# Kernel tuning notes

Hardware: AMD Instinct MI355X
Metric: run time of the kernel (lower is better)

## Reference

```python
import jax, jax.numpy as jnp
import numpy as np

K = 8          # circulant block size
H = 16         # heads


def circ_linear(x, w, b):
    """Block-circulant linear. x: [..., in], w: [p, q, K] (first column of each
    KxK circulant block), b: [p*K]. y[p] = sum_q circ(w[p,q]) @ x_block[q],
    computed as circular convolution via rFFT."""
    q = w.shape[1]
    xb = x.reshape(x.shape[:-1] + (q, K))            # [..., q, K]
    Fx = jnp.fft.rfft(xb, axis=-1)                    # [..., q, K//2+1]
    Fw = jnp.fft.rfft(w, axis=-1)                     # [p, q, K//2+1]
    Fy = jnp.einsum('pqf,...qf->...pf', Fw, Fx)
    y = jnp.fft.irfft(Fy, n=K, axis=-1)               # [..., p, K]
    return y.reshape(x.shape[:-1] + (-1,)) + b


def setup_inputs() -> dict:
    key = jax.random.key(0)
    ks = jax.random.split(key, 9)
    B, N, D = 2, 1024, 1024
    p = q = D // K
    std = 1.0 / np.sqrt(D)
    mk = lambda k: jax.random.normal(k, (p, q, K), dtype=jnp.float32) * std
    mb = lambda k: jax.random.normal(k, (D,), dtype=jnp.float32) * 0.01
    x = jax.random.normal(ks[0], (B, N, D), dtype=jnp.float32)
    # causal mask: True = masked out
    mask = (~jnp.tril(jnp.ones((N, N), dtype=bool)))[None, None]  # [1,1,N,N]
    return {
        'x': x, 'mask': mask,
        'wq': mk(ks[1]), 'bq': mb(ks[2]),
        'wk': mk(ks[3]), 'bk': mb(ks[4]),
        'wv': mk(ks[5]), 'bv': mb(ks[6]),
        'wo': mk(ks[7]), 'bo': mb(ks[8]),
    }


def reference(x, mask, wq, bq, wk, bk, wv, bv, wo, bo):
    B, N, D = x.shape
    dh = D // H
    heads = lambda a: a.reshape(B, N, H, dh).transpose(0, 2, 1, 3)  # [B,H,N,dh]
    qh = heads(circ_linear(x, wq, bq))
    kh = heads(circ_linear(x, wk, bk))
    vh = heads(circ_linear(x, wv, bv))
    attn = jnp.einsum('bhnd,bhmd->bhnm', qh, kh)
    attn = jnp.where(mask, -jnp.inf, attn)
    probs = jax.nn.softmax(attn / jnp.sqrt(jnp.float32(dh)), axis=-1)
    out = jnp.einsum('bhnm,bhmd->bhnd', probs, vh)
    out = out.transpose(0, 2, 1, 3).reshape(B, N, D)
    return circ_linear(out, wo, bo)
```

## Files before the change

kernel.cpp:

```cpp
#include <hip/hip_runtime.h>
#include <hip/hip_bf16.h>

#define DIM   1024
#define NSEQ  1024
#define BATCH 2
#define NHEAD 16
#define DH    64

typedef unsigned short u16;
typedef __attribute__((ext_vector_type(8))) short  short8;
typedef __attribute__((ext_vector_type(4))) float  f32x4;
typedef __attribute__((ext_vector_type(8))) unsigned short u16x8;
typedef __attribute__((ext_vector_type(4))) unsigned short u16x4;

#define EXP_SCALE 0.18033688011112042f
#define SLOT 4352

__device__ __forceinline__ u16 f2bf(float f) {
  union { float f; unsigned u; } v; v.f = f;
  unsigned r = v.u + 0x7FFFu + ((v.u >> 16) & 1u);
  return (u16)(r >> 16);
}

#define GLD(src, dst)                                                          \
  __builtin_amdgcn_global_load_lds(                                           \
      (const __attribute__((address_space(1))) void*)(src),                   \
      (__attribute__((address_space(3))) void*)(dst), 16, 0, 0)

__global__ __launch_bounds__(256) void prep_bf16(
    const float* __restrict__ wq, const float* __restrict__ wk,
    const float* __restrict__ wv, const float* __restrict__ wo,
    const float* __restrict__ x,
    u16* __restrict__ Wd, u16* __restrict__ Xb) {
  const int bid = blockIdx.x;
  if (bid < 2048) {
    const int z = bid >> 9;
    const float* w = (z == 0) ? wq : (z == 1) ? wk : (z == 2) ? wv : wo;
    u16* out = Wd + (size_t)z * DIM * DIM;
    const int idx8 = (bid & 511) * 256 + threadIdx.x;
    const int r = idx8 >> 7;
    const int q = idx8 & 127;
    const int p = r >> 3, a = r & 7;
    const float* wrow = w + (size_t)(p * 128 + q) * 8;
    const float4 w0 = *(const float4*)(wrow);
    const float4 w1 = *(const float4*)(wrow + 4);
    const float wv8[8] = {w0.x, w0.y, w0.z, w0.w, w1.x, w1.y, w1.z, w1.w};
    u16x8 o;
#pragma unroll
    for (int j = 0; j < 8; ++j) o[j] = f2bf(wv8[(a - j) & 7]);
    ((u16x8*)out)[idx8] = o;
  } else {
    const int i = (bid - 2048) * 256 + threadIdx.x;
    const float4 a = ((const float4*)x)[2 * i];
    const float4 b = ((const float4*)x)[2 * i + 1];
    u16x8 o;
    o[0] = f2bf(a.x); o[1] = f2bf(a.y); o[2] = f2bf(a.z); o[3] = f2bf(a.w);
    o[4] = f2bf(b.x); o[5] = f2bf(b.y); o[6] = f2bf(b.z); o[7] = f2bf(b.w);
    ((u16x8*)Xb)[i] = o;
  }
}

__global__ __launch_bounds__(256, 2) void gemm_qkv(
    const u16* __restrict__ A, const u16* __restrict__ Wd,
    const float* __restrict__ bq, const float* __restrict__ bk,
    const float* __restrict__ bv,
    u16* __restrict__ Qb, u16* __restrict__ Kb, u16* __restrict__ Vt) {
  __shared__ u16 As[2][64 * 64];
  __shared__ u16 Bs[2][3 * 64 * 64];

  const int tid  = threadIdx.x;
  const int w    = tid >> 6, lane = tid & 63;
  const int nb   = blockIdx.x * 64;
  const int mb   = blockIdx.y * 64;

  f32x4 acc[3][2][2] = {};

  const int m0 = (w >> 1) * 32, n0 = (w & 1) * 32;
  const int lr = lane & 15, lg = lane >> 4;
  const int lsw = lr & 7;

#define STAGE(buf, k0)                                                         \
  do {                                                                         \
    _Pragma("unroll")                                                          \
    for (int i = 0; i < 2; ++i) {                                              \
      const int bc = i * 256 + w * 64;                                         \
      const int c  = bc + lane;                                                \
      const int row = c >> 3, js = (c & 7) ^ (row & 7);                        \
      GLD(A + (size_t)(mb + row) * DIM + (k0) + js * 8, As[buf] + bc * 8);     \
    }                                                                          \
    _Pragma("unroll")                                                          \
    for (int i = 0; i < 6; ++i) {                                              \
      const int bc = i * 256 + w * 64;                                         \
      const int c  = bc + lane;                                                \
      const int z  = c >> 9, ci = c & 511;                                     \
      const int row = ci >> 3, js = (ci & 7) ^ (row & 7);                      \
      GLD(Wd + (size_t)z * DIM * DIM + (size_t)(nb + row) * DIM + (k0) + js * 8,\
          Bs[buf] + bc * 8);                                                   \
    }                                                                          \
  } while (0)

  STAGE(0, 0);
  __syncthreads();
  int cur = 0;
  for (int k0 = 0; k0 < DIM; k0 += 64) {
    if (k0 + 64 < DIM) STAGE(cur ^ 1, k0 + 64);

#pragma unroll
    for (int kk = 0; kk < 2; ++kk) {
      const int sw = ((kk * 4 + lg) ^ lsw) * 8;
      short8 a[2], b[3][2];
#pragma unroll
      for (int mi = 0; mi < 2; ++mi)
        a[mi] = *(const short8*)&As[cur][(m0 + mi * 16 + lr) * 64 + sw];
#pragma unroll
      for (int z = 0; z < 3; ++z)
#pragma unroll
        for (int ni = 0; ni < 2; ++ni)
          b[z][ni] = *(const short8*)
              &Bs[cur][z * 4096 + (n0 + ni * 16 + lr) * 64 + sw];
#pragma unroll
      for (int z = 0; z < 3; ++z)
#pragma unroll
        for (int mi = 0; mi < 2; ++mi)
#pragma unroll
          for (int ni = 0; ni < 2; ++ni)
            acc[z][mi][ni] = __builtin_amdgcn_mfma_f32_16x16x32_bf16(
                a[mi], b[z][ni], acc[z][mi][ni], 0, 0, 0);
    }

    __syncthreads();
    cur ^= 1;
  }
#undef STAGE

  const int col = lane & 15, rq4 = (lane >> 4) * 4;

#pragma unroll
  for (int z = 0; z < 2; ++z) {
    u16* C = z ? Kb : Qb;
    const float* bias = z ? bk : bq;
#pragma unroll
    for (int ni = 0; ni < 2; ++ni) {
      const int gc = nb + n0 + ni * 16 + col;
      const float bb = bias[gc];
#pragma unroll
      for (int mi = 0; mi < 2; ++mi) {
        const size_t rbase = (size_t)(mb + m0 + mi * 16 + rq4) * DIM + gc;
#pragma unroll
        for (int j = 0; j < 4; ++j)
          C[rbase + (size_t)j * DIM] = f2bf(acc[z][mi][ni][j] + bb);
      }
    }
  }
  {
    const int b = mb >> 10;
    const int h = blockIdx.x;
    const int nbase = (mb & (NSEQ - 1)) + m0;
#pragma unroll
    for (int ni = 0; ni < 2; ++ni) {
      const int dh = n0 + ni * 16 + col;
      const float bb = bv[nb + dh];
      u16* vrow = Vt + ((size_t)(b * NHEAD + h) * DH + dh) * NSEQ;
#pragma unroll
      for (int mi = 0; mi < 2; ++mi) {
        const int nn = nbase + mi * 16 + rq4;
        u16x4 o;
#pragma unroll
        for (int j = 0; j < 4; ++j) o[j] = f2bf(acc[2][mi][ni][j] + bb);
        *(u16x4*)(vrow + nn) = o;
      }
    }
  }
}

__global__ __launch_bounds__(256, 2) void gemm_o(
    const u16* __restrict__ A, const u16* __restrict__ W,
    const float* __restrict__ bias, float* __restrict__ C) {
  __shared__ u16 As[2][64 * 64];
  __shared__ u16 Bs[2][64 * 64];

  const int tid  = threadIdx.x;
  const int w    = tid >> 6, lane = tid & 63;
  const int mb   = blockIdx.y * 64, nb = blockIdx.x * 64;

  f32x4 acc[2][2] = {};

  const int m0 = (w >> 1) * 32, n0 = (w & 1) * 32;
  const int lr = lane & 15, lg = lane >> 4;
  const int lsw = lr & 7;

#define STAGE(buf, k0)                                                         \
  do {                                                                         \
    _Pragma("unroll")                                                          \
    for (int i = 0; i < 2; ++i) {                                              \
      const int bc = i * 256 + w * 64;                                         \
      const int c  = bc + lane;                                                \
      const int row = c >> 3, js = (c & 7) ^ (row & 7);                        \
      GLD(A + (size_t)(mb + row) * DIM + (k0) + js * 8, As[buf] + bc * 8);     \
      GLD(W + (size_t)(nb + row) * DIM + (k0) + js * 8, Bs[buf] + bc * 8);     \
    }                                                                          \
  } while (0)

  STAGE(0, 0);
  __syncthreads();
  int cur = 0;
  for (int k0 = 0; k0 < DIM; k0 += 64) {
    if (k0 + 64 < DIM) STAGE(cur ^ 1, k0 + 64);

#pragma unroll
    for (int kk = 0; kk < 2; ++kk) {
      const int sw = ((kk * 4 + lg) ^ lsw) * 8;
      short8 a[2], b[2];
#pragma unroll
      for (int mi = 0; mi < 2; ++mi)
        a[mi] = *(const short8*)&As[cur][(m0 + mi * 16 + lr) * 64 + sw];
#pragma unroll
      for (int ni = 0; ni < 2; ++ni)
        b[ni] = *(const short8*)&Bs[cur][(n0 + ni * 16 + lr) * 64 + sw];
#pragma unroll
      for (int mi = 0; mi < 2; ++mi)
#pragma unroll
        for (int ni = 0; ni < 2; ++ni)
          acc[mi][ni] = __builtin_amdgcn_mfma_f32_16x16x32_bf16(
              a[mi], b[ni], acc[mi][ni], 0, 0, 0);
    }

    __syncthreads();
    cur ^= 1;
  }
#undef STAGE

  const int col = lane & 15, rq = (lane >> 4) * 4;
#pragma unroll
  for (int ni = 0; ni < 2; ++ni) {
    const int gc = nb + n0 + ni * 16 + col;
    const float bv = bias[gc];
#pragma unroll
    for (int mi = 0; mi < 2; ++mi) {
      const size_t rbase = (size_t)(mb + m0 + mi * 16 + rq) * DIM + gc;
#pragma unroll
      for (int j = 0; j < 4; ++j)
        C[rbase + (size_t)j * DIM] = acc[mi][ni][j] + bv;
    }
  }
}

__global__ __launch_bounds__(256, 4) void attn_split(
    const u16* __restrict__ Qg, const u16* __restrict__ Kg,
    const u16* __restrict__ Vt, float* __restrict__ Part,
    u16* __restrict__ AOb) {
  const int bid = blockIdx.x;
  const int s   = bid >> 3;
  const int g   = (bid & 7) * 4 + s / 40;
  const int b   = g >> 4, h = g & 15;
  int idx = s % 40, qt = 0, cc = 0;
  for (int t = 15; t >= 0; --t) {
    const int nc = (t >> 2) + 1;
    if (idx < nc) { qt = t; cc = idx; break; }
    idx -= nc;
  }
  const int tid = threadIdx.x;
  const int w  = tid >> 6, l = tid & 63;
  const int lr = l & 15, lg = l >> 4;

  __shared__ u16 Klds[4][64 * 64];
  __shared__ u16 Vlds[4][64 * 64];
  __shared__ u16 Plds[4][16 * 64];

  const int qg = qt * 64 + w * 16 + lr;
  const size_t base_bh = (size_t)b * NSEQ * DIM + (size_t)h * DH;
  const size_t vt_bh   = (size_t)(b * NHEAD + h) * DH * NSEQ;

  short8 qf[2];
#pragma unroll
  for (int c = 0; c < 2; ++c)
    qf[c] = *(const short8*)(Qg + base_bh + (size_t)qg * DIM + c * 32 + lg * 8);

  f32x4 acc_o[4] = {};
  float m_run = -1e30f, l_run = 0.f;
  char* pbase = (char*)Plds[w];
  const int psw = (lr & 7) << 4;

  const int srow8 = l >> 3;
  const int sj    = l & 7;

  const int kt0 = cc * 4;
  const int nt  = min(kt0 + 4, qt + 1) - kt0;

#pragma unroll
  for (int t = 0; t < 4; ++t) {
    if (t < nt) {
      const int kt = kt0 + t;
#pragma unroll
      for (int i = 0; i < 2; ++i) {
        const int cb  = w * 2 + i;
        const int row = cb * 8 + srow8;
        const int c16 = sj ^ (row & 7);
        GLD(Kg + base_bh + (size_t)(kt * 64 + row) * DIM + c16 * 8,
            Klds[t] + cb * 512);
        GLD(Vt + vt_bh + (size_t)row * NSEQ + kt * 64 + c16 * 8,
            Vlds[t] + cb * 512);
      }
    }
  }
  __syncthreads();

  for (int it = 0; it < nt; ++it) {
    const int kt = kt0 + it;

    f32x4 s4[4] = {};
#pragma unroll
    for (int t16 = 0; t16 < 4; ++t16) {
      const int row = t16 * 16 + lr;
#pragma unroll
      for (int c = 0; c < 2; ++c) {
        const int c16 = (c * 4 + lg) ^ (row & 7);
        const short8 kf = *(const short8*)
            ((const char*)Klds[it] + row * 128 + c16 * 16);
        s4[t16] = __builtin_amdgcn_mfma_f32_16x16x32_bf16(kf, qf[c], s4[t16], 0, 0, 0);
      }
    }

    const bool diag = (kt == qt);
    float mloc = -1e30f;
#pragma unroll
    for (int t16 = 0; t16 < 4; ++t16)
#pragma unroll
      for (int j = 0; j < 4; ++j) {
        float v = s4[t16][j];
        if (diag && (kt * 64 + t16 * 16 + lg * 4 + j) > qg) v = -1e30f;
        s4[t16][j] = v;
        mloc = fmaxf(mloc, v);
      }
    mloc = fmaxf(mloc, __shfl_xor(mloc, 16));
    mloc = fmaxf(mloc, __shfl_xor(mloc, 32));
    const float m_new = fmaxf(m_run, mloc);
    const float a = exp2f((m_run - m_new) * EXP_SCALE);
    float psum = 0.f;
    u16x4 pk[4];
#pragma unroll
    for (int t16 = 0; t16 < 4; ++t16)
#pragma unroll
      for (int j = 0; j < 4; ++j) {
        const float p = exp2f((s4[t16][j] - m_new) * EXP_SCALE);
        psum += p;
        pk[t16][j] = f2bf(p);
      }
    psum += __shfl_xor(psum, 16);
    psum += __shfl_xor(psum, 32);
    l_run = l_run * a + psum;
    m_run = m_new;
#pragma unroll
    for (int d = 0; d < 4; ++d) acc_o[d] *= a;

#pragma unroll
    for (int t16 = 0; t16 < 4; ++t16)
      *(u16x4*)(pbase + lr * 128 + ((t16 * 32 + lg * 8) ^ psw)) = pk[t16];

#pragma unroll
    for (int c = 0; c < 2; ++c) {
      const short8 pf = *(const short8*)
          (pbase + lr * 128 + ((c * 64 + lg * 16) ^ psw));
#pragma unroll
      for (int d = 0; d < 4; ++d) {
        const int dh = d * 16 + lr;
        const int c16 = (c * 4 + lg) ^ (dh & 7);
        const short8 vf = *(const short8*)
            ((const char*)Vlds[it] + dh * 128 + c16 * 16);
        acc_o[d] = __builtin_amdgcn_mfma_f32_16x16x32_bf16(vf, pf, acc_o[d], 0, 0, 0);
      }
    }
  }

  const int ql = w * 16 + lr;
  if (qt < 4) {
    const float inv = 1.f / l_run;
    u16* Op = AOb + (size_t)(b * NSEQ + qt * 64 + ql) * DIM + (size_t)h * DH;
#pragma unroll
    for (int d = 0; d < 4; ++d) {
      u16x4 o;
      o[0] = f2bf(acc_o[d][0] * inv); o[1] = f2bf(acc_o[d][1] * inv);
      o[2] = f2bf(acc_o[d][2] * inv); o[3] = f2bf(acc_o[d][3] * inv);
      *(u16x4*)(Op + d * 16 + lg * 4) = o;
    }
  } else {
    float* slot = Part + (((size_t)(b * NHEAD + h) * 16 + qt) * 4 + cc) * SLOT;
#pragma unroll
    for (int d = 0; d < 4; ++d)
      *(f32x4*)(slot + ql * 64 + d * 16 + lg * 4) = acc_o[d];
    if (lg == 0) {
      slot[4096 + ql] = m_run;
      slot[4160 + ql] = l_run;
    }
  }
}

__global__ __launch_bounds__(256) void attn_merge(
    const float* __restrict__ Part, u16* __restrict__ AOb) {
  const int qt = blockIdx.x + 4, h = blockIdx.y, b = blockIdx.z;
  const int t = threadIdx.x;
  const int q = t >> 2, quad = t & 3;
  const int nc = (qt >> 2) + 1;
  const float* base = Part + ((size_t)(b * NHEAD + h) * 16 + qt) * 4 * SLOT;

  float mv[4], lv[4];
  float M = -1e30f;
  for (int c = 0; c < nc; ++c) {
    mv[c] = base[c * SLOT + 4096 + q];
    lv[c] = base[c * SLOT + 4160 + q];
    M = fmaxf(M, mv[c]);
  }
  float L = 0.f, fc[4];
  for (int c = 0; c < nc; ++c) {
    fc[c] = exp2f((mv[c] - M) * EXP_SCALE);
    L += lv[c] * fc[c];
  }
  const float inv = 1.f / L;

  float o[16] = {};
  for (int c = 0; c < nc; ++c) {
    const float* op = base + c * SLOT + q * 64 + quad * 16;
    const float f = fc[c];
#pragma unroll
    for (int i = 0; i < 4; ++i) {
      const f32x4 v = *(const f32x4*)(op + i * 4);
      o[i * 4 + 0] += f * v[0]; o[i * 4 + 1] += f * v[1];
      o[i * 4 + 2] += f * v[2]; o[i * 4 + 3] += f * v[3];
    }
  }

  u16* dst = AOb + (size_t)(b * NSEQ + qt * 64 + q) * DIM + h * DH + quad * 16;
  u16x8 o0, o1;
#pragma unroll
  for (int i = 0; i < 8; ++i) { o0[i] = f2bf(o[i] * inv); o1[i] = f2bf(o[8 + i] * inv); }
  *(u16x8*)(dst)     = o0;
  *(u16x8*)(dst + 8) = o1;
}

extern "C" void kernel_launch(void* const* d_in, const int* in_sizes, int n_in,
                              void* d_out, int out_size, void* d_ws, size_t ws_size,
                              hipStream_t stream) {
  const float* x  = (const float*)d_in[0];
  const float* wq = (const float*)d_in[2];
  const float* bq = (const float*)d_in[3];
  const float* wk = (const float*)d_in[4];
  const float* bk = (const float*)d_in[5];
  const float* wv = (const float*)d_in[6];
  const float* bv = (const float*)d_in[7];
  const float* wo = (const float*)d_in[8];
  const float* bo = (const float*)d_in[9];

  char* ws = (char*)d_ws;
  u16* Wd    = (u16*)(ws);
  u16* Xb    = (u16*)(ws + ((size_t)8  << 20));
  u16* Qb    = (u16*)(ws + ((size_t)12 << 20));
  u16* Kb    = (u16*)(ws + ((size_t)16 << 20));
  u16* Vt    = (u16*)(ws + ((size_t)24 << 20));
  u16* AOb   = (u16*)(ws + ((size_t)28 << 20));
  float* Prt = (float*)(ws + ((size_t)32 << 20));

  prep_bf16<<<dim3(3072, 1, 1), 256, 0, stream>>>(wq, wk, wv, wo, x, Wd, Xb);

  gemm_qkv<<<dim3(NHEAD, (BATCH * NSEQ) / 64, 1), 256, 0, stream>>>(
      Xb, Wd, bq, bk, bv, Qb, Kb, Vt);

  attn_split<<<dim3(1280, 1, 1), 256, 0, stream>>>(Qb, Kb, Vt, Prt, AOb);

  attn_merge<<<dim3(12, NHEAD, BATCH), 256, 0, stream>>>(Prt, AOb);

  gemm_o<<<dim3(DIM / 64, (BATCH * NSEQ) / 64, 1), 256, 0, stream>>>(
      AOb, Wd + (size_t)3 * DIM * DIM, bo, (float*)d_out);
}
```

Measured before the change: 73.85 us.

## Split attention KV into 3-tile chunks and pass P via lane permutes instead of LDS

Changes the split-K attention partition from 4 KV tiles per block to 3, raising the block count and reducing per-block LDS, and updates the partial-slot layout and merge kernel to match. Also removes the per-wave LDS round trip for the probability matrix, converting to bf16 with packed converts and rearranging fragments via permlane swaps directly in registers. The goal is better load balance and occupancy plus fewer LDS writes and reads. The cost is more partial outputs to merge and more launched blocks.

New measurement: 72.84 us. About the same (-1.4%).

```diff
diff --git a/kernel.cpp b/kernel.cpp
--- a/kernel.cpp
+++ b/kernel.cpp
@@ -245,17 +245,17 @@
   }
 }
 
-__global__ __launch_bounds__(256, 4) void attn_split(
+__global__ __launch_bounds__(256, 3) void attn_split(
     const u16* __restrict__ Qg, const u16* __restrict__ Kg,
     const u16* __restrict__ Vt, float* __restrict__ Part,
     u16* __restrict__ AOb) {
   const int bid = blockIdx.x;
   const int s   = bid >> 3;
-  const int g   = (bid & 7) * 4 + s / 40;
+  const int g   = (bid & 7) * 4 + s / 51;
   const int b   = g >> 4, h = g & 15;
-  int idx = s % 40, qt = 0, cc = 0;
+  int idx = s % 51, qt = 0, cc = 0;
   for (int t = 15; t >= 0; --t) {
-    const int nc = (t >> 2) + 1;
+    const int nc = t / 3 + 1;
     if (idx < nc) { qt = t; cc = idx; break; }
     idx -= nc;
   }
@@ -263,9 +263,8 @@
   const int w  = tid >> 6, l = tid & 63;
   const int lr = l & 15, lg = l >> 4;
 
-  __shared__ u16 Klds[4][64 * 64];
-  __shared__ u16 Vlds[4][64 * 64];
-  __shared__ u16 Plds[4][16 * 64];
+  __shared__ u16 Klds[3][64 * 64];
+  __shared__ u16 Vlds[3][64 * 64];
 
   const int qg = qt * 64 + w * 16 + lr;
   const size_t base_bh = (size_t)b * NSEQ * DIM + (size_t)h * DH;
@@ -278,17 +277,15 @@
 
   f32x4 acc_o[4] = {};
   float m_run = -1e30f, l_run = 0.f;
-  char* pbase = (char*)Plds[w];
-  const int psw = (lr & 7) << 4;
 
   const int srow8 = l >> 3;
   const int sj    = l & 7;
 
-  const int kt0 = cc * 4;
-  const int nt  = min(kt0 + 4, qt + 1) - kt0;
-
-#pragma unroll
-  for (int t = 0; t < 4; ++t) {
+  const int kt0 = cc * 3;
+  const int nt  = min(kt0 + 3, qt + 1) - kt0;
+
+#pragma unroll
+  for (int t = 0; t < 3; ++t) {
     if (t < nt) {
       const int kt = kt0 + t;
 #pragma unroll
@@ -337,14 +334,13 @@
     const float m_new = fmaxf(m_run, mloc);
     const float a = exp2f((m_run - m_new) * EXP_SCALE);
     float psum = 0.f;
-    u16x4 pk[4];
 #pragma unroll
     for (int t16 = 0; t16 < 4; ++t16)
 #pragma unroll
       for (int j = 0; j < 4; ++j) {
         const float p = exp2f((s4[t16][j] - m_new) * EXP_SCALE);
         psum += p;
-        pk[t16][j] = f2bf(p);
+        s4[t16][j] = p;
       }
     psum += __shfl_xor(psum, 16);
     psum += __shfl_xor(psum, 32);
@@ -354,13 +350,23 @@
     for (int d = 0; d < 4; ++d) acc_o[d] *= a;
 
 #pragma unroll
-    for (int t16 = 0; t16 < 4; ++t16)
-      *(u16x4*)(pbase + lr * 128 + ((t16 * 32 + lg * 8) ^ psw)) = pk[t16];
-
-#pragma unroll
     for (int c = 0; c < 2; ++c) {
-      const short8 pf = *(const short8*)
-          (pbase + lr * 128 + ((c * 64 + lg * 16) ^ psw));
+      unsigned a0, a1, b0, b1;
+      asm("v_cvt_pk_bf16_f32 %0, %1, %2"
+          : "=v"(a0) : "v"(s4[2 * c][0]), "v"(s4[2 * c][1]));
+      asm("v_cvt_pk_bf16_f32 %0, %1, %2"
+          : "=v"(a1) : "v"(s4[2 * c][2]), "v"(s4[2 * c][3]));
+      asm("v_cvt_pk_bf16_f32 %0, %1, %2"
+          : "=v"(b0) : "v"(s4[2 * c + 1][0]), "v"(s4[2 * c + 1][1]));
+      asm("v_cvt_pk_bf16_f32 %0, %1, %2"
+          : "=v"(b1) : "v"(s4[2 * c + 1][2]), "v"(s4[2 * c + 1][3]));
+      asm("v_permlane32_swap_b32 %0, %1" : "+v"(a0), "+v"(b0));
+      asm("v_permlane16_swap_b32 %0, %1" : "+v"(a0), "+v"(b0));
+      asm("v_permlane32_swap_b32 %0, %1" : "+v"(a1), "+v"(b1));
+      asm("v_permlane16_swap_b32 %0, %1" : "+v"(a1), "+v"(b1));
+      union { unsigned u[4]; short8 s; } pu;
+      pu.u[0] = a0; pu.u[1] = a1; pu.u[2] = b0; pu.u[3] = b1;
+      const short8 pf = pu.s;
 #pragma unroll
       for (int d = 0; d < 4; ++d) {
         const int dh = d * 16 + lr;
@@ -373,7 +379,7 @@
   }
 
   const int ql = w * 16 + lr;
-  if (qt < 4) {
+  if (qt < 3) {
     const float inv = 1.f / l_run;
     u16* Op = AOb + (size_t)(b * NSEQ + qt * 64 + ql) * DIM + (size_t)h * DH;
 #pragma unroll
@@ -384,7 +390,7 @@
       *(u16x4*)(Op + d * 16 + lg * 4) = o;
     }
   } else {
-    float* slot = Part + (((size_t)(b * NHEAD + h) * 16 + qt) * 4 + cc) * SLOT;
+    float* slot = Part + (((size_t)(b * NHEAD + h) * 16 + qt) * 6 + cc) * SLOT;
 #pragma unroll
     for (int d = 0; d < 4; ++d)
       *(f32x4*)(slot + ql * 64 + d * 16 + lg * 4) = acc_o[d];
@@ -397,20 +403,20 @@
 
 __global__ __launch_bounds__(256) void attn_merge(
     const float* __restrict__ Part, u16* __restrict__ AOb) {
-  const int qt = blockIdx.x + 4, h = blockIdx.y, b = blockIdx.z;
+  const int qt = blockIdx.x + 3, h = blockIdx.y, b = blockIdx.z;
   const int t = threadIdx.x;
   const int q = t >> 2, quad = t & 3;
-  const int nc = (qt >> 2) + 1;
-  const float* base = Part + ((size_t)(b * NHEAD + h) * 16 + qt) * 4 * SLOT;
-
-  float mv[4], lv[4];
+  const int nc = qt / 3 + 1;
+  const float* base = Part + ((size_t)(b * NHEAD + h) * 16 + qt) * 6 * SLOT;
+
+  float mv[6], lv[6], fc[6];
   float M = -1e30f;
   for (int c = 0; c < nc; ++c) {
     mv[c] = base[c * SLOT + 4096 + q];
     lv[c] = base[c * SLOT + 4160 + q];
     M = fmaxf(M, mv[c]);
   }
-  float L = 0.f, fc[4];
+  float L = 0.f;
   for (int c = 0; c < nc; ++c) {
     fc[c] = exp2f((mv[c] - M) * EXP_SCALE);
     L += lv[c] * fc[c];
@@ -464,9 +470,9 @@
   gemm_qkv<<<dim3(NHEAD, (BATCH * NSEQ) / 64, 1), 256, 0, stream>>>(
       Xb, Wd, bq, bk, bv, Qb, Kb, Vt);
 
-  attn_split<<<dim3(1280, 1, 1), 256, 0, stream>>>(Qb, Kb, Vt, Prt, AOb);
-
-  attn_merge<<<dim3(12, NHEAD, BATCH), 256, 0, stream>>>(Prt, AOb);
+  attn_split<<<dim3(1632, 1, 1), 256, 0, stream>>>(Qb, Kb, Vt, Prt, AOb);
+
+  attn_merge<<<dim3(13, NHEAD, BATCH), 256, 0, stream>>>(Prt, AOb);
 
   gemm_o<<<dim3(DIM / 64, (BATCH * NSEQ) / 64, 1), 256, 0, stream>>>(
       AOb, Wd + (size_t)3 * DIM * DIM, bo, (float*)d_out);
```
